# Optimization experiments

Measured on AMD Instinct MI355X. Metric: run time of the kernel, lower is better.

## Reference

```python
import jax, jax.numpy as jnp
import numpy as np

D_MODEL = 2048
D_HEAD = 128
NUM_HEADS = 16
D_KV_LATENT = 512
BATCH = 2
SEQ = 2048


def setup_inputs() -> dict:
    key = jax.random.key(0)
    ks = jax.random.split(key, 6)
    s = 0.02
    return {
        "x": jax.random.normal(ks[0], (BATCH, SEQ, D_MODEL), jnp.float32),
        "Wd": jax.random.normal(ks[1], (D_KV_LATENT, D_MODEL), jnp.float32) * s,
        "Wuk": jax.random.normal(ks[2], (NUM_HEADS * D_HEAD, D_KV_LATENT), jnp.float32) * s,
        "Wuv": jax.random.normal(ks[3], (NUM_HEADS * D_HEAD, D_KV_LATENT), jnp.float32) * s,
        "Wq": jax.random.normal(ks[4], (NUM_HEADS * D_HEAD, D_MODEL), jnp.float32) * s,
        "Wo": jax.random.normal(ks[5], (D_MODEL, NUM_HEADS * D_HEAD), jnp.float32) * s,
        "use_cache": 1,
    }


def _mla_cache_path(x, Wd, Wuk, Wuv, Wq, Wo):
    # Weight-absorbed MLA prefill from an empty cache (total_seq_len == seq_len).
    b, s, dm = x.shape
    h, dh, c = NUM_HEADS, D_HEAD, D_KV_LATENT
    # latents = downsample(x): [b, s, c]
    latents = jnp.einsum("bsm,cm->bsc", x, Wd)
    # absorbed weights: q_uk [h, dm, c], out_uv [h, dm, c]
    q_uk = jnp.einsum("hdm,hdc->hmc", Wq.reshape(h, dh, dm), Wuk.reshape(h, dh, c))
    out_uv = jnp.einsum("mhd,hdc->hmc", Wo.reshape(dm, h, dh), Wuv.reshape(h, dh, c))
    # query_part: [b, h, s, c]
    query_part = jnp.einsum("bsm,hmc->bhsc", x, q_uk)
    # value_part: [b, h, s, dm]
    value_part = jnp.einsum("hmc,btc->bhtm", out_uv, latents)
    # scores over latent dim: [b, h, s, s]
    scores = jnp.einsum("bhsc,btc->bhst", query_part, latents) / np.sqrt(dh).astype(np.float32)
    causal = jnp.triu(jnp.ones((s, s), dtype=bool), k=1)
    scores = jnp.where(causal, -jnp.inf, scores)
    attn = jax.nn.softmax(scores, axis=-1)
    # output already in model dim; sum contributions over heads
    out = jnp.einsum("bhst,bhtm->bsm", attn, value_part)
    return out


def reference(x, Wd, Wuk, Wuv, Wq, Wo, use_cache):
    # use_cache is a static Python int (1 -> weight-absorbed cache path)
    return _mla_cache_path(x, Wd, Wuk, Wuv, Wq, Wo)
```

## Files before the change

kernel.cpp:

```cpp
#include <hip/hip_runtime.h>
#include <hip/hip_bf16.h>

typedef __attribute__((ext_vector_type(8))) short short8x;
typedef __attribute__((ext_vector_type(4))) float f32x4;

__device__ __forceinline__ ushort f2bf(float f){
  union { __hip_bfloat16 b; ushort u; } cvt;
  cvt.b = __float2bfloat16(f);
  return cvt.u;
}

__global__ __launch_bounds__(256) void cvt_kernel(const float* __restrict__ in, ushort* __restrict__ out, long n){
  long i = ((long)blockIdx.x * 256 + threadIdx.x) * 4;
  if (i >= n) return;
  float4 v = *(const float4*)(in + i);
  ushort4 o;
  o.x = f2bf(v.x); o.y = f2bf(v.y); o.z = f2bf(v.z); o.w = f2bf(v.w);
  *(ushort4*)(out + i) = o;
}

template<int OUTBF>
__global__ __launch_bounds__(256, 3)
void gemm_bt(const ushort* __restrict__ A, const ushort* __restrict__ BT, void* __restrict__ Cv,
             int M, int N, int K, int lda, int ldb, int ldc,
             long aZ, long bZ, long cZ, float scale)
{
  __shared__ __align__(16) ushort As[2][128 * 32];
  __shared__ __align__(16) ushort Bs[2][128 * 32];
  const int z = blockIdx.z;
  const ushort* Ab = A + (long)z * aZ;
  const ushort* Bb = BT + (long)z * bZ;
  const int tid = threadIdx.x, lane = tid & 63, w = tid >> 6;
  const int wm = w >> 1, wn = w & 1;
  const int lq = lane & 15, q4 = lane >> 4;

  int lin = blockIdx.x + gridDim.x * blockIdx.y;
  const int cpx = (gridDim.x * gridDim.y) >> 3;
  lin = (lin & 7) * cpx + (lin >> 3);
  const int bx = lin % gridDim.x, by = lin / gridDim.x;

  const long arow = (long)by * 128, brow = (long)bx * 128;
  const int lr = lane >> 2, lc = (lane & 3) * 8;

  const f32x4 z4 = {0.f, 0.f, 0.f, 0.f};
  f32x4 acc[4][4];
#pragma unroll
  for (int i = 0; i < 4; i++)
#pragma unroll
    for (int j = 0; j < 4; j++) acc[i][j] = z4;

  auto stage = [&](int buf, int k0){
#pragma unroll
    for (int is = 0; is < 2; ++is){
      const int rb = is * 64 + w * 16;
      const ushort* ga = Ab + (arow + rb + lr) * (long)lda + k0 + lc;
      const ushort* gb = Bb + (brow + rb + lr) * (long)ldb + k0 + lc;
      __builtin_amdgcn_global_load_lds((const __attribute__((address_space(1))) void*)ga,
                                       (__attribute__((address_space(3))) void*)&As[buf][rb * 32], 16, 0, 0);
      __builtin_amdgcn_global_load_lds((const __attribute__((address_space(1))) void*)gb,
                                       (__attribute__((address_space(3))) void*)&Bs[buf][rb * 32], 16, 0, 0);
    }
  };

  const int nk = K >> 5;
  stage(0, 0);
  for (int kt = 0; kt < nk; ++kt){
    __syncthreads();
    if (kt + 1 < nk) stage((kt + 1) & 1, (kt + 1) * 32);
    const int buf = kt & 1;
    short8x a[4], b[4];
#pragma unroll
    for (int i = 0; i < 4; i++){
      a[i] = *(const short8x*)&As[buf][(wm * 64 + i * 16 + lq) * 32 + q4 * 8];
      b[i] = *(const short8x*)&Bs[buf][(wn * 64 + i * 16 + lq) * 32 + q4 * 8];
    }
#pragma unroll
    for (int i = 0; i < 4; i++)
#pragma unroll
      for (int j = 0; j < 4; j++)
        acc[i][j] = __builtin_amdgcn_mfma_f32_16x16x32_bf16(a[i], b[j], acc[i][j], 0, 0, 0);
  }

  const long crowb = arow + wm * 64;
  const long ccolb = brow + wn * 64;
#pragma unroll
  for (int i = 0; i < 4; i++)
#pragma unroll
    for (int j = 0; j < 4; j++)
#pragma unroll
      for (int r = 0; r < 4; r++){
        const long row = crowb + i * 16 + q4 * 4 + r;
        const long col = ccolb + j * 16 + lq;
        const float v = acc[i][j][r] * scale;
        if (OUTBF) ((ushort*)Cv)[(long)z * cZ + row * ldc + col] = f2bf(v);
        else       ((float*)Cv)[(long)z * cZ + row * ldc + col] = v;
      }
}

__global__ __launch_bounds__(256, 1)
void flash6_kernel(const ushort* __restrict__ q, const ushort* __restrict__ k,
                   const ushort* __restrict__ vT, ushort* __restrict__ attnO)
{
  __shared__ __align__(16) ushort Kb[2][32 * 128];
  __shared__ __align__(16) ushort Vb[2][128 * 32];
  __shared__ __align__(16) ushort Pl[4][32][40];

  const int tid = threadIdx.x, lane = tid & 63, w = tid >> 6;
  const int lq = lane & 15, q4 = lane >> 4;

  const int xcd = blockIdx.x & 7, g = blockIdx.x >> 3;
  const int bh = xcd * 4 + (g & 3);
  const int strip = 15 - (g >> 2);
  const int b = bh & 1, h = bh >> 1;

  const int nt = 4 * strip + 4;
  const int wdiag = 4 * strip + w;

  const ushort* kb_ = k + (long)b * 2048 * 2048 + h * 128;
  const ushort* vb_ = vT + (long)h * 128 * 4096 + (long)b * 2048;

  const ushort* kbase[2]; const ushort* vbase[2]; int kofs[2], vofs[2];
#pragma unroll
  for (int is = 0; is < 2; ++is){
    const int ofse = is * 2048 + w * 512;
    const int row = (ofse >> 7) + (lane >> 4);
    const int gsw = (lane & 15) ^ (row & 7);
    kbase[is] = kb_ + (long)row * 2048 + gsw * 8;
    kofs[is] = ofse;
    const int drow = (ofse >> 5) + (lane >> 2);
    vbase[is] = vb_ + (long)drow * 4096 + (lane & 3) * 8;
    vofs[is] = ofse;
  }

  auto stage = [&](int buf, int tt){
    const long t0 = (long)tt * 32;
#pragma unroll
    for (int is = 0; is < 2; ++is){
      __builtin_amdgcn_global_load_lds((const __attribute__((address_space(1))) void*)(kbase[is] + t0 * 2048),
          (__attribute__((address_space(3))) void*)&Kb[buf][kofs[is]], 16, 0, 0);
      __builtin_amdgcn_global_load_lds((const __attribute__((address_space(1))) void*)(vbase[is] + t0),
          (__attribute__((address_space(3))) void*)&Vb[buf][vofs[is]], 16, 0, 0);
    }
  };

  const f32x4 z4 = {0.f, 0.f, 0.f, 0.f};

  const int qrow0 = strip * 128 + w * 32;
  const long qgbase = (long)b * 2048 + qrow0;

  short8x qf[2][4];
#pragma unroll
  for (int si = 0; si < 2; si++){
    const ushort* qp = q + (qgbase + si * 16 + lq) * 2048 + h * 128 + q4 * 8;
#pragma unroll
    for (int ks = 0; ks < 4; ks++) qf[si][ks] = *(const short8x*)(qp + ks * 32);
  }

  f32x4 oacc[8][2];
#pragma unroll
  for (int dt = 0; dt < 8; dt++){ oacc[dt][0] = z4; oacc[dt][1] = z4; }
  float dsum0 = 0.f, dsum1 = 0.f;

  stage(0, 0);
  stage(1, 1);

#pragma unroll 1
  for (int tt = 0; tt < nt; ++tt){
    if (tt == nt - 1) asm volatile("s_waitcnt vmcnt(0)" ::: "memory");
    else              asm volatile("s_waitcnt vmcnt(4)" ::: "memory");
    __syncthreads();
    const int cur = tt & 1;

    if (tt <= wdiag){
      short8x ak[2][4];
#pragma unroll
      for (int ti = 0; ti < 2; ti++){
        const int r = ti * 16 + lq;
        const int rb = r * 128;
        const int rx = r & 7;
#pragma unroll
        for (int ks = 0; ks < 4; ks++)
          ak[ti][ks] = *(const short8x*)&Kb[cur][rb + (((ks * 4 + q4) ^ rx) * 8)];
      }
      f32x4 st[2][2] = {{z4, z4}, {z4, z4}};
#pragma unroll
      for (int ks = 0; ks < 4; ks++)
#pragma unroll
        for (int ti = 0; ti < 2; ti++)
#pragma unroll
          for (int si = 0; si < 2; si++)
            st[ti][si] = __builtin_amdgcn_mfma_f32_16x16x32_bf16(ak[ti][ks], qf[si][ks], st[ti][si], 0, 0, 0);

      const bool diag = (tt == wdiag);
#pragma unroll
      for (int ti = 0; ti < 2; ti++)
#pragma unroll
        for (int si = 0; si < 2; si++){
          ushort4 pb;
#pragma unroll
          for (int r = 0; r < 4; r++){
            const int tl = ti * 16 + q4 * 4 + r;
            const int sl = si * 16 + lq;
            float p = __expf(st[ti][si][r]);
            if (diag && tl > sl) p = 0.f;
            if (si) dsum1 += p; else dsum0 += p;
            ((ushort*)&pb)[r] = f2bf(p);
          }
          *(ushort4*)&Pl[w][si * 16 + lq][ti * 16 + q4 * 4] = pb;
        }
      asm volatile("s_waitcnt lgkmcnt(0)" ::: "memory");
      __builtin_amdgcn_sched_barrier(0);
      short8x pf0 = *(const short8x*)&Pl[w][lq][q4 * 8];
      short8x pf1 = *(const short8x*)&Pl[w][16 + lq][q4 * 8];
      __builtin_amdgcn_sched_barrier(0);
#pragma unroll
      for (int dt = 0; dt < 8; dt++){
        const short8x av = *(const short8x*)&Vb[cur][(dt * 16 + lq) * 32 + q4 * 8];
        oacc[dt][0] = __builtin_amdgcn_mfma_f32_16x16x32_bf16(av, pf0, oacc[dt][0], 0, 0, 0);
        oacc[dt][1] = __builtin_amdgcn_mfma_f32_16x16x32_bf16(av, pf1, oacc[dt][1], 0, 0, 0);
      }
    }
    __syncthreads();
    if (tt + 2 < nt) stage(cur, tt + 2);
  }

  dsum0 += __shfl_xor(dsum0, 16); dsum0 += __shfl_xor(dsum0, 32);
  dsum1 += __shfl_xor(dsum1, 16); dsum1 += __shfl_xor(dsum1, 32);
  const float inv0 = 1.f / dsum0, inv1 = 1.f / dsum1;

#pragma unroll
  for (int dt = 0; dt < 8; dt++)
#pragma unroll
    for (int si = 0; si < 2; si++){
      const float inv = si ? inv1 : inv0;
      ushort4 o;
      o.x = f2bf(oacc[dt][si][0] * inv);
      o.y = f2bf(oacc[dt][si][1] * inv);
      o.z = f2bf(oacc[dt][si][2] * inv);
      o.w = f2bf(oacc[dt][si][3] * inv);
      *(ushort4*)(attnO + (qgbase + si * 16 + lq) * 2048 + h * 128 + dt * 16 + q4 * 4) = o;
    }
}

extern "C" void kernel_launch(void* const* d_in, const int* in_sizes, int n_in,
                              void* d_out, int out_size, void* d_ws, size_t ws_size,
                              hipStream_t stream)
{
  const float* x   = (const float*)d_in[0];
  const float* Wd  = (const float*)d_in[1];
  const float* Wuk = (const float*)d_in[2];
  const float* Wuv = (const float*)d_in[3];
  const float* Wq  = (const float*)d_in[4];
  const float* Wo  = (const float*)d_in[5];
  float* out = (float*)d_out;
  ushort* ws = (ushort*)d_ws;

  ushort* xb    = ws + 0L;
  ushort* wdb   = ws + 8388608L;
  ushort* wqb   = ws + 9437184L;
  ushort* wob   = ws + 13631488L;
  ushort* wukb  = ws + 17825792L;
  ushort* wuvb  = ws + 18874368L;
  ushort* lat   = ws + 19922944L;
  ushort* qb    = ws + 22020096L;
  ushort* kb    = ws + 30408704L;
  ushort* vTb   = ws + 38797312L;
  ushort* attnO = ws + 47185920L;

  cvt_kernel<<<8192, 256, 0, stream>>>(x,   xb,   8388608L);
  cvt_kernel<<<1024, 256, 0, stream>>>(Wd,  wdb,  1048576L);
  cvt_kernel<<<4096, 256, 0, stream>>>(Wq,  wqb,  4194304L);
  cvt_kernel<<<4096, 256, 0, stream>>>(Wo,  wob,  4194304L);
  cvt_kernel<<<1024, 256, 0, stream>>>(Wuk, wukb, 1048576L);
  cvt_kernel<<<1024, 256, 0, stream>>>(Wuv, wuvb, 1048576L);

  gemm_bt<1><<<dim3(4, 32, 1), 256, 0, stream>>>(xb, wdb, lat, 4096, 512, 2048,
      2048, 2048, 512, 0L, 0L, 0L, 1.0f);
  gemm_bt<1><<<dim3(16, 32, 1), 256, 0, stream>>>(xb, wqb, qb, 4096, 2048, 2048,
      2048, 2048, 2048, 0L, 0L, 0L, 0.08838834764831845f);
  gemm_bt<1><<<dim3(16, 32, 1), 256, 0, stream>>>(lat, wukb, kb, 4096, 2048, 512,
      512, 512, 2048, 0L, 0L, 0L, 1.0f);
  gemm_bt<1><<<dim3(32, 16, 1), 256, 0, stream>>>(wuvb, lat, vTb, 2048, 4096, 512,
      512, 512, 4096, 0L, 0L, 0L, 1.0f);
  flash6_kernel<<<512, 256, 0, stream>>>(qb, kb, vTb, attnO);
  gemm_bt<0><<<dim3(16, 32, 1), 256, 0, stream>>>(attnO, wob, out, 4096, 2048, 2048,
      2048, 2048, 2048, 0L, 0L, 0L, 1.0f);
}
```

Before: 277.3 us.

## Enlarge flash attention tiles to 64-key blocks with 8-wave workgroups

Replaces the 4-wave, 128-row-query flash kernel with an 8-wave, 256-query-row kernel that stages 64-key K/V tiles, so each staged tile is reused by twice as many waves. V tiles in shared memory gain an XOR swizzle, and P is written and consumed per 16-row subtile. The grid halves to 256 blocks, and the order no longer schedules heavy causal strips first, which may worsen load imbalance across CUs.

```diff
diff --git a/kernel.cpp b/kernel.cpp
--- a/kernel.cpp
+++ b/kernel.cpp
@@ -97,24 +97,25 @@
       }
 }
 
-__global__ __launch_bounds__(256, 1)
-void flash6_kernel(const ushort* __restrict__ q, const ushort* __restrict__ k,
+__global__ __launch_bounds__(512, 2)
+void flash7_kernel(const ushort* __restrict__ q, const ushort* __restrict__ k,
                    const ushort* __restrict__ vT, ushort* __restrict__ attnO)
 {
-  __shared__ __align__(16) ushort Kb[2][32 * 128];
-  __shared__ __align__(16) ushort Vb[2][128 * 32];
-  __shared__ __align__(16) ushort Pl[4][32][40];
+  __shared__ __align__(16) ushort Kb[2][64 * 128];
+  __shared__ __align__(16) ushort Vb[2][128 * 64];
+  __shared__ __align__(16) ushort Pl[8][2][16][72];
 
   const int tid = threadIdx.x, lane = tid & 63, w = tid >> 6;
   const int lq = lane & 15, q4 = lane >> 4;
 
-  const int xcd = blockIdx.x & 7, g = blockIdx.x >> 3;
-  const int bh = xcd * 4 + (g & 3);
-  const int strip = 15 - (g >> 2);
+  const int xcd = blockIdx.x & 7;
+  const int bh = xcd * 4 + ((blockIdx.x >> 3) & 3);
+  const int qb = blockIdx.x >> 5;
   const int b = bh & 1, h = bh >> 1;
 
-  const int nt = 4 * strip + 4;
-  const int wdiag = 4 * strip + w;
+  const int nt = (qb + 1) * 4;
+  const int wd = qb * 4 + (w >> 1);
+  const int moff = (w & 1) * 32;
 
   const ushort* kb_ = k + (long)b * 2048 * 2048 + h * 128;
   const ushort* vb_ = vT + (long)h * 128 * 4096 + (long)b * 2048;
@@ -122,18 +123,19 @@
   const ushort* kbase[2]; const ushort* vbase[2]; int kofs[2], vofs[2];
 #pragma unroll
   for (int is = 0; is < 2; ++is){
-    const int ofse = is * 2048 + w * 512;
-    const int row = (ofse >> 7) + (lane >> 4);
-    const int gsw = (lane & 15) ^ (row & 7);
-    kbase[is] = kb_ + (long)row * 2048 + gsw * 8;
+    const int ofse = is * 4096 + w * 512;
+    const int krow = (ofse >> 7) + (lane >> 4);
+    const int kg = (lane & 15) ^ (krow & 7);
+    kbase[is] = kb_ + (long)krow * 2048 + kg * 8;
     kofs[is] = ofse;
-    const int drow = (ofse >> 5) + (lane >> 2);
-    vbase[is] = vb_ + (long)drow * 4096 + (lane & 3) * 8;
+    const int drow = (ofse >> 6) + (lane >> 3);
+    const int vg = (lane & 7) ^ (drow & 7);
+    vbase[is] = vb_ + (long)drow * 4096 + vg * 8;
     vofs[is] = ofse;
   }
 
   auto stage = [&](int buf, int tt){
-    const long t0 = (long)tt * 32;
+    const long t0 = (long)tt * 64;
 #pragma unroll
     for (int is = 0; is < 2; ++is){
       __builtin_amdgcn_global_load_lds((const __attribute__((address_space(1))) void*)(kbase[is] + t0 * 2048),
@@ -145,7 +147,7 @@
 
   const f32x4 z4 = {0.f, 0.f, 0.f, 0.f};
 
-  const int qrow0 = strip * 128 + w * 32;
+  const int qrow0 = qb * 256 + w * 32;
   const long qgbase = (long)b * 2048 + qrow0;
 
   short8x qf[2][4];
@@ -171,10 +173,10 @@
     __syncthreads();
     const int cur = tt & 1;
 
-    if (tt <= wdiag){
-      short8x ak[2][4];
-#pragma unroll
-      for (int ti = 0; ti < 2; ti++){
+    if (tt <= wd){
+      short8x ak[4][4];
+#pragma unroll
+      for (int ti = 0; ti < 4; ti++){
         const int r = ti * 16 + lq;
         const int rb = r * 128;
         const int rx = r & 7;
@@ -182,42 +184,48 @@
         for (int ks = 0; ks < 4; ks++)
           ak[ti][ks] = *(const short8x*)&Kb[cur][rb + (((ks * 4 + q4) ^ rx) * 8)];
       }
-      f32x4 st[2][2] = {{z4, z4}, {z4, z4}};
+      f32x4 st[4][2];
+#pragma unroll
+      for (int ti = 0; ti < 4; ti++){ st[ti][0] = z4; st[ti][1] = z4; }
 #pragma unroll
       for (int ks = 0; ks < 4; ks++)
 #pragma unroll
-        for (int ti = 0; ti < 2; ti++)
+        for (int ti = 0; ti < 4; ti++)
 #pragma unroll
           for (int si = 0; si < 2; si++)
             st[ti][si] = __builtin_amdgcn_mfma_f32_16x16x32_bf16(ak[ti][ks], qf[si][ks], st[ti][si], 0, 0, 0);
 
-      const bool diag = (tt == wdiag);
-#pragma unroll
-      for (int ti = 0; ti < 2; ti++)
-#pragma unroll
-        for (int si = 0; si < 2; si++){
+      const bool diag = (tt == wd);
+#pragma unroll
+      for (int si = 0; si < 2; si++){
+#pragma unroll
+        for (int ti = 0; ti < 4; ti++){
           ushort4 pb;
 #pragma unroll
           for (int r = 0; r < 4; r++){
             const int tl = ti * 16 + q4 * 4 + r;
-            const int sl = si * 16 + lq;
             float p = __expf(st[ti][si][r]);
-            if (diag && tl > sl) p = 0.f;
+            if (diag && tl > moff + si * 16 + lq) p = 0.f;
             if (si) dsum1 += p; else dsum0 += p;
             ((ushort*)&pb)[r] = f2bf(p);
           }
-          *(ushort4*)&Pl[w][si * 16 + lq][ti * 16 + q4 * 4] = pb;
+          *(ushort4*)&Pl[w][si][lq][ti * 16 + q4 * 4] = pb;
         }
-      asm volatile("s_waitcnt lgkmcnt(0)" ::: "memory");
-      __builtin_amdgcn_sched_barrier(0);
-      short8x pf0 = *(const short8x*)&Pl[w][lq][q4 * 8];
-      short8x pf1 = *(const short8x*)&Pl[w][16 + lq][q4 * 8];
-      __builtin_amdgcn_sched_barrier(0);
-#pragma unroll
-      for (int dt = 0; dt < 8; dt++){
-        const short8x av = *(const short8x*)&Vb[cur][(dt * 16 + lq) * 32 + q4 * 8];
-        oacc[dt][0] = __builtin_amdgcn_mfma_f32_16x16x32_bf16(av, pf0, oacc[dt][0], 0, 0, 0);
-        oacc[dt][1] = __builtin_amdgcn_mfma_f32_16x16x32_bf16(av, pf1, oacc[dt][1], 0, 0, 0);
+        asm volatile("s_waitcnt lgkmcnt(0)" ::: "memory");
+        __builtin_amdgcn_sched_barrier(0);
+        const short8x pf0 = *(const short8x*)&Pl[w][si][lq][q4 * 8];
+        const short8x pf1 = *(const short8x*)&Pl[w][si][lq][32 + q4 * 8];
+        __builtin_amdgcn_sched_barrier(0);
+#pragma unroll
+        for (int dt = 0; dt < 8; dt++){
+          const int r = dt * 16 + lq;
+          const int rb = r * 64;
+          const int rx = lq & 7;
+          const short8x av0 = *(const short8x*)&Vb[cur][rb + (((0 * 4 + q4) ^ rx) * 8)];
+          const short8x av1 = *(const short8x*)&Vb[cur][rb + (((1 * 4 + q4) ^ rx) * 8)];
+          oacc[dt][si] = __builtin_amdgcn_mfma_f32_16x16x32_bf16(av0, pf0, oacc[dt][si], 0, 0, 0);
+          oacc[dt][si] = __builtin_amdgcn_mfma_f32_16x16x32_bf16(av1, pf1, oacc[dt][si], 0, 0, 0);
+        }
       }
     }
     __syncthreads();
@@ -282,7 +290,7 @@
       512, 512, 2048, 0L, 0L, 0L, 1.0f);
   gemm_bt<1><<<dim3(32, 16, 1), 256, 0, stream>>>(wuvb, lat, vTb, 2048, 4096, 512,
       512, 512, 4096, 0L, 0L, 0L, 1.0f);
-  flash6_kernel<<<512, 256, 0, stream>>>(qb, kb, vTb, attnO);
+  flash7_kernel<<<256, 512, 0, stream>>>(qb, kb, vTb, attnO);
   gemm_bt<0><<<dim3(16, 32, 1), 256, 0, stream>>>(attnO, wob, out, 4096, 2048, 2048,
       2048, 2048, 2048, 0L, 0L, 0L, 1.0f);
 }
```

New measurement: 278.2 us. About the same (+0.3%).
